# Optimization experiments

Hardware: AMD Instinct MI355X
Metric: run time of the kernel (lower is better)

The kernel has to match this reference:

```python
import jax, jax.numpy as jnp
import numpy as np

N_LAYERS = 3
NUM_NODES = 400000
EMB_DIM = 64
N_EDGES = 4000000


def setup_inputs() -> dict:
    key = jax.random.key(0)
    k1, k2, k3, k4 = jax.random.split(key, 4)
    embedding = jax.random.normal(k1, (NUM_NODES, EMB_DIM), dtype=jnp.float32) * 0.1
    adj_row = jax.random.randint(k2, (N_EDGES,), 0, NUM_NODES, dtype=jnp.int64)
    adj_col = jax.random.randint(k3, (N_EDGES,), 0, NUM_NODES, dtype=jnp.int64)
    # normalized adjacency values (e.g. 1/sqrt(d_i d_j)); positive, small
    adj_val = jax.random.uniform(k4, (N_EDGES,), dtype=jnp.float32) * 0.01
    return {"embedding": embedding, "adj_row": adj_row, "adj_col": adj_col, "adj_val": adj_val}


def _spmm(row, col, val, x):
    # sparse [N,N] @ dense [N,D]: gather neighbor rows, scale, scatter-add
    msgs = val[:, None] * x[col]                      # [E, D]
    return jax.ops.segment_sum(msgs, row, num_segments=NUM_NODES)


def reference(embedding, adj_row, adj_col, adj_val):
    # LightGCN propagation: running mean over layer outputs (fused accumulator,
    # mathematically identical to stack+mean over n_layers+1 embeddings)
    x = embedding
    acc = x
    for _ in range(N_LAYERS):
        x = _spmm(adj_row, adj_col, adj_val, x)
        acc = acc + x
    all_embeddings = acc / jnp.asarray(N_LAYERS + 1, dtype=x.dtype)
    return all_embeddings
```

## Files before the change

### kernel.cpp

```cpp
#include <hip/hip_runtime.h>

#define EMB 64
#define SCAN_B 256
#define RPB 32
#define RPW 8
#define ECAP 1024

typedef unsigned uint2v __attribute__((ext_vector_type(2)));
typedef float float4v __attribute__((ext_vector_type(4)));

__device__ inline uint2 nt_load_u2(const uint2* p) {
    uint2v v = __builtin_nontemporal_load((const uint2v*)p);
    return make_uint2(v.x, v.y);
}
__device__ inline void nt_store_u2(uint2* p, uint2 v) {
    uint2v t; t.x = v.x; t.y = v.y;
    __builtin_nontemporal_store(t, (uint2v*)p);
}
__device__ inline float4 nt_load_f4(const float4* p) {
    float4v v = __builtin_nontemporal_load((const float4v*)p);
    return make_float4(v.x, v.y, v.z, v.w);
}
__device__ inline void nt_store_f4(float4* p, float4 v) {
    float4v t; t.x = v.x; t.y = v.y; t.z = v.z; t.w = v.w;
    __builtin_nontemporal_store(t, (float4v*)p);
}

__device__ inline unsigned short f2bf(float f) {
    unsigned u = __float_as_uint(f);
    return (unsigned short)((u + 0x7fffu + ((u >> 16) & 1u)) >> 16);
}
__device__ inline float bl(unsigned u) { return __uint_as_float(u << 16); }
__device__ inline float bh(unsigned u) { return __uint_as_float(u & 0xffff0000u); }


__global__ void zero_ints(int* __restrict__ p, int n) {
    int i = blockIdx.x * blockDim.x + threadIdx.x;
    if (i < n) p[i] = 0;
}

__global__ void hist_rows(const int* __restrict__ row, int* __restrict__ S, int E) {
    int e = blockIdx.x * blockDim.x + threadIdx.x;
    if (e < E) atomicAdd(&S[__builtin_nontemporal_load(row + e)], 1);
}

__global__ void scan_block_sums(const int* __restrict__ S, int* __restrict__ bsum, int N) {
    __shared__ int sdata[SCAN_B];
    int i = blockIdx.x * SCAN_B + threadIdx.x;
    sdata[threadIdx.x] = (i < N) ? S[i] : 0;
    __syncthreads();
    for (int off = SCAN_B / 2; off > 0; off >>= 1) {
        if (threadIdx.x < off) sdata[threadIdx.x] += sdata[threadIdx.x + off];
        __syncthreads();
    }
    if (threadIdx.x == 0) bsum[blockIdx.x] = sdata[0];
}

__global__ void scan_sums(int* __restrict__ bsum, int nb) {
    __shared__ int part[1024];
    int t = threadIdx.x;
    int i0 = 2 * t, i1 = 2 * t + 1;
    int a = (i0 < nb) ? bsum[i0] : 0;
    int b = (i1 < nb) ? bsum[i1] : 0;
    part[t] = a + b;
    __syncthreads();
    for (int off = 1; off < 1024; off <<= 1) {
        int v = part[t];
        int add = (t >= off) ? part[t - off] : 0;
        __syncthreads();
        part[t] = v + add;
        __syncthreads();
    }
    int excl = (t == 0) ? 0 : part[t - 1];
    if (i0 < nb) bsum[i0] = excl;
    if (i1 < nb) bsum[i1] = excl + a;
}

__global__ void scan_apply(int* __restrict__ S, const int* __restrict__ bsum, int N) {
    __shared__ int sdata[SCAN_B];
    int i = blockIdx.x * SCAN_B + threadIdx.x;
    int v = (i < N) ? S[i] : 0;
    sdata[threadIdx.x] = v;
    __syncthreads();
    for (int off = 1; off < SCAN_B; off <<= 1) {
        int val = sdata[threadIdx.x];
        int add = (threadIdx.x >= off) ? sdata[threadIdx.x - off] : 0;
        __syncthreads();
        sdata[threadIdx.x] = val + add;
        __syncthreads();
    }
    int excl = (threadIdx.x == 0 ? 0 : sdata[threadIdx.x - 1]) + bsum[blockIdx.x];
    if (i < N) S[i] = excl;
}

__global__ void scatter_edges_ranged(const int* __restrict__ row, const int* __restrict__ col,
                                     const float* __restrict__ val,
                                     int* __restrict__ S, uint2* __restrict__ epack,
                                     int E, int rstep) {
    int pass  = blockIdx.x & 7;
    int chunk = blockIdx.x >> 3;
    int e = chunk * blockDim.x + threadIdx.x;
    if (e >= E) return;
    int r = __builtin_nontemporal_load(row + e);
    int lo = pass * rstep;
    if (r < lo || r >= lo + rstep) return;
    int c = __builtin_nontemporal_load(col + e);
    float v = __builtin_nontemporal_load(val + e);
    int pos = atomicAdd(&S[r], 1);
    epack[pos] = make_uint2((unsigned)c, __float_as_uint(v));
}

__global__ void conv_bf16(const float4* __restrict__ src, uint2* __restrict__ dst, int n4) {
    int i = blockIdx.x * blockDim.x + threadIdx.x;
    if (i < n4) {
        float4 v = nt_load_f4(src + i);
        unsigned w0 = (unsigned)f2bf(v.x) | ((unsigned)f2bf(v.y) << 16);
        unsigned w1 = (unsigned)f2bf(v.z) | ((unsigned)f2bf(v.w) << 16);
        nt_store_u2(dst + i, make_uint2(w0, w1));
    }
}

template<bool STG>
__device__ __forceinline__ void spmm_rows(
    const uint2* __restrict__ epack, const uint2* __restrict__ esh, int beg0,
    const int* __restrict__ Ssh, int j0,
    const unsigned short* __restrict__ x, const float* __restrict__ emb,
    unsigned short* __restrict__ y, float* __restrict__ acc,
    int rb, int N, int mode, int lane, int grp, int d4)
{
    const uint2 z2 = make_uint2(0u, 0u);

#define EDG(i) (STG ? esh[(i) - beg0] : epack[i])
#define LOADR(J, B_, E_, P0, P1, P2, P3, G0, G1, G2, G3)                         \
    {                                                                            \
        B_ = Ssh[J]; E_ = Ssh[(J) + 1];                                          \
        int i0 = B_ + grp, i1 = i0 + 4, i2 = i0 + 8, i3 = i0 + 12;               \
        P0 = (i0 < E_) ? EDG(i0) : z2;                                           \
        P1 = (i1 < E_) ? EDG(i1) : z2;                                           \
        P2 = (i2 < E_) ? EDG(i2) : z2;                                           \
        P3 = (i3 < E_) ? EDG(i3) : z2;                                           \
        G0 = (i0 < E_) ? ((const uint2*)(x + ((size_t)P0.x << 6)))[d4] : z2;     \
        G1 = (i1 < E_) ? ((const uint2*)(x + ((size_t)P1.x << 6)))[d4] : z2;     \
        G2 = (i2 < E_) ? ((const uint2*)(x + ((size_t)P2.x << 6)))[d4] : z2;     \
        G3 = (i3 < E_) ? ((const uint2*)(x + ((size_t)P3.x << 6)))[d4] : z2;     \
    }

    int aB = 0, aE = 0;
    uint2 ap0 = z2, ap1 = z2, ap2 = z2, ap3 = z2, ag0 = z2, ag1 = z2, ag2 = z2, ag3 = z2;
    int bB = 0, bE = 0;
    uint2 bp0 = z2, bp1 = z2, bp2 = z2, bp3 = z2, bg0 = z2, bg1 = z2, bg2 = z2, bg3 = z2;

    LOADR(j0, aB, aE, ap0, ap1, ap2, ap3, ag0, ag1, ag2, ag3);

    for (int k = 0; k < RPW; ++k) {
        int j = j0 + k;
        int r = rb + j;
        if (k + 1 < RPW) {
            LOADR(j + 1, bB, bE, bp0, bp1, bp2, bp3, bg0, bg1, bg2, bg3);
        }

        float4 s = make_float4(0.f, 0.f, 0.f, 0.f);
        {
            int i0 = aB + grp, i1 = i0 + 4, i2 = i0 + 8, i3 = i0 + 12;
            float w0 = (i0 < aE) ? __uint_as_float(ap0.y) : 0.f;
            float w1 = (i1 < aE) ? __uint_as_float(ap1.y) : 0.f;
            float w2 = (i2 < aE) ? __uint_as_float(ap2.y) : 0.f;
            float w3 = (i3 < aE) ? __uint_as_float(ap3.y) : 0.f;
            s.x += w0 * bl(ag0.x); s.y += w0 * bh(ag0.x); s.z += w0 * bl(ag0.y); s.w += w0 * bh(ag0.y);
            s.x += w1 * bl(ag1.x); s.y += w1 * bh(ag1.x); s.z += w1 * bl(ag1.y); s.w += w1 * bh(ag1.y);
            s.x += w2 * bl(ag2.x); s.y += w2 * bh(ag2.x); s.z += w2 * bl(ag2.y); s.w += w2 * bh(ag2.y);
            s.x += w3 * bl(ag3.x); s.y += w3 * bh(ag3.x); s.z += w3 * bl(ag3.y); s.w += w3 * bh(ag3.y);
        }
        for (int base = aB + 16; base < aE; base += 16) {
            int i0 = base + grp, i1 = i0 + 4, i2 = i0 + 8, i3 = i0 + 12;
            uint2 p0 = (i0 < aE) ? EDG(i0) : z2;
            uint2 p1 = (i1 < aE) ? EDG(i1) : z2;
            uint2 p2 = (i2 < aE) ? EDG(i2) : z2;
            uint2 p3 = (i3 < aE) ? EDG(i3) : z2;
            uint2 g0 = (i0 < aE) ? ((const uint2*)(x + ((size_t)p0.x << 6)))[d4] : z2;
            uint2 g1 = (i1 < aE) ? ((const uint2*)(x + ((size_t)p1.x << 6)))[d4] : z2;
            uint2 g2 = (i2 < aE) ? ((const uint2*)(x + ((size_t)p2.x << 6)))[d4] : z2;
            uint2 g3 = (i3 < aE) ? ((const uint2*)(x + ((size_t)p3.x << 6)))[d4] : z2;
            float w0 = (i0 < aE) ? __uint_as_float(p0.y) : 0.f;
            float w1 = (i1 < aE) ? __uint_as_float(p1.y) : 0.f;
            float w2 = (i2 < aE) ? __uint_as_float(p2.y) : 0.f;
            float w3 = (i3 < aE) ? __uint_as_float(p3.y) : 0.f;
            s.x += w0 * bl(g0.x); s.y += w0 * bh(g0.x); s.z += w0 * bl(g0.y); s.w += w0 * bh(g0.y);
            s.x += w1 * bl(g1.x); s.y += w1 * bh(g1.x); s.z += w1 * bl(g1.y); s.w += w1 * bh(g1.y);
            s.x += w2 * bl(g2.x); s.y += w2 * bh(g2.x); s.z += w2 * bl(g2.y); s.w += w2 * bh(g2.y);
            s.x += w3 * bl(g3.x); s.y += w3 * bh(g3.x); s.z += w3 * bl(g3.y); s.w += w3 * bh(g3.y);
        }

        s.x += __shfl_xor(s.x, 32); s.y += __shfl_xor(s.y, 32);
        s.z += __shfl_xor(s.z, 32); s.w += __shfl_xor(s.w, 32);
        s.x += __shfl_xor(s.x, 16); s.y += __shfl_xor(s.y, 16);
        s.z += __shfl_xor(s.z, 16); s.w += __shfl_xor(s.w, 16);

        if (lane < 16 && r < N) {
            size_t o4 = (size_t)r * 16 + d4;
            if (mode != 2) {
                unsigned w0 = (unsigned)f2bf(s.x) | ((unsigned)f2bf(s.y) << 16);
                unsigned w1 = (unsigned)f2bf(s.z) | ((unsigned)f2bf(s.w) << 16);
                nt_store_u2(((uint2*)y) + o4, make_uint2(w0, w1));
            }
            if (mode == 0) {
                float4 e4 = nt_load_f4(((const float4*)emb) + o4);
                nt_store_f4(((float4*)acc) + o4,
                            make_float4(e4.x + s.x, e4.y + s.y, e4.z + s.z, e4.w + s.w));
            } else if (mode == 1) {
                float4 a4 = nt_load_f4(((const float4*)acc) + o4);
                nt_store_f4(((float4*)acc) + o4,
                            make_float4(a4.x + s.x, a4.y + s.y, a4.z + s.z, a4.w + s.w));
            } else if (mode == 2) {
                float4 a4 = nt_load_f4(((const float4*)acc) + o4);
                nt_store_f4(((float4*)acc) + o4,
                            make_float4((a4.x + s.x) * 0.25f, (a4.y + s.y) * 0.25f,
                                        (a4.z + s.z) * 0.25f, (a4.w + s.w) * 0.25f));
            }
        }
        aB = bB; aE = bE;
        ap0 = bp0; ap1 = bp1; ap2 = bp2; ap3 = bp3;
        ag0 = bg0; ag1 = bg1; ag2 = bg2; ag3 = bg3;
    }
#undef LOADR
#undef EDG
}

__global__ __launch_bounds__(256) void spmm_csr2(
    const uint2* __restrict__ epack, const int* __restrict__ S,
    const unsigned short* __restrict__ x, const float* __restrict__ emb,
    unsigned short* __restrict__ y, float* __restrict__ acc,
    int N, int mode)
{
    __shared__ int Ssh[RPB + 1];
    __shared__ uint2 esh[ECAP];

    int tid = threadIdx.x;
    int rb = blockIdx.x * RPB;

    if (tid <= RPB) {
        int rr = rb - 1 + tid;
        Ssh[tid] = (rr < 0) ? 0 : S[rr < N ? rr : (N - 1)];
    }
    __syncthreads();

    int beg0 = Ssh[0];
    int nE = Ssh[RPB] - beg0;
    bool staged = (nE <= ECAP);
    if (staged) {
        for (int i = tid; i < nE; i += 256) esh[i] = nt_load_u2(epack + beg0 + i);
    }
    __syncthreads();

    int wid = tid >> 6, lane = tid & 63;
    int grp = lane >> 4, d4 = lane & 15;
    int j0 = wid * RPW;

    if (staged)
        spmm_rows<true >(epack, esh, beg0, Ssh, j0, x, emb, y, acc, rb, N, mode, lane, grp, d4);
    else
        spmm_rows<false>(epack, esh, beg0, Ssh, j0, x, emb, y, acc, rb, N, mode, lane, grp, d4);
}


__global__ void lgcn_init(const float4* __restrict__ emb, float4* __restrict__ A,
                          float4* __restrict__ acc, float4* __restrict__ B, int n4) {
    int i = blockIdx.x * blockDim.x + threadIdx.x;
    if (i < n4) { float4 v = emb[i]; A[i] = v; acc[i] = v; B[i] = make_float4(0,0,0,0); }
}
__global__ void lgcn_spmm(const int* __restrict__ row, const int* __restrict__ col,
                          const float* __restrict__ val, const float* __restrict__ x,
                          float* __restrict__ y, int E) {
    int gid = blockIdx.x * blockDim.x + threadIdx.x;
    int e = gid >> 6;
    if (e >= E) return;
    int d = threadIdx.x & 63;
    atomicAdd(y + (size_t)row[e] * EMB + d, val[e] * x[(size_t)col[e] * EMB + d]);
}
__global__ void lgcn_addzero(float4* __restrict__ acc, const float4* __restrict__ X,
                             float4* __restrict__ Y, int n4) {
    int i = blockIdx.x * blockDim.x + threadIdx.x;
    if (i < n4) {
        float4 a = acc[i]; float4 xv = X[i];
        a.x += xv.x; a.y += xv.y; a.z += xv.z; a.w += xv.w;
        acc[i] = a; Y[i] = make_float4(0,0,0,0);
    }
}
__global__ void lgcn_final(float4* __restrict__ acc, const float4* __restrict__ X, int n4) {
    int i = blockIdx.x * blockDim.x + threadIdx.x;
    if (i < n4) {
        float4 a = acc[i]; float4 xv = X[i];
        a.x = (a.x + xv.x) * 0.25f; a.y = (a.y + xv.y) * 0.25f;
        a.z = (a.z + xv.z) * 0.25f; a.w = (a.w + xv.w) * 0.25f;
        acc[i] = a;
    }
}

extern "C" void kernel_launch(void* const* d_in, const int* in_sizes, int n_in,
                              void* d_out, int out_size, void* d_ws, size_t ws_size,
                              hipStream_t stream) {
    const float* emb = (const float*)d_in[0];
    const int*   row = (const int*)d_in[1];
    const int*   col = (const int*)d_in[2];
    const float* val = (const float*)d_in[3];
    float* acc = (float*)d_out;

    const int N = in_sizes[0] / EMB;
    const int E = in_sizes[1];
    const int TB = 256;

    const size_t buf_elems = (size_t)N * EMB;
    const int nb = (N + SCAN_B - 1) / SCAN_B;

    const size_t need = (size_t)E * 8 + buf_elems * 2 * 3 + (size_t)N * 4 + (size_t)nb * 4;

    if (ws_size >= need) {
        uint2* epack = (uint2*)d_ws;
        unsigned short* X0 = (unsigned short*)(epack + E);
        unsigned short* X1 = X0 + buf_elems;
        unsigned short* X2 = X1 + buf_elems;
        int* S    = (int*)(X2 + buf_elems);
        int* bsum = S + N;

        const int eb  = (E + TB - 1) / TB;
        const int nbN = (N + TB - 1) / TB;
        const int n4  = (int)(buf_elems / 4);
        const int cvb = (n4 + TB - 1) / TB;
        const int spmm_blocks = (N + RPB - 1) / RPB;
        const int rstep = (N + 7) / 8;

        zero_ints<<<nbN, TB, 0, stream>>>(S, N);
        hist_rows<<<eb, TB, 0, stream>>>(row, S, E);
        scan_block_sums<<<nb, SCAN_B, 0, stream>>>(S, bsum, N);
        scan_sums<<<1, 1024, 0, stream>>>(bsum, nb);
        scan_apply<<<nb, SCAN_B, 0, stream>>>(S, bsum, N);
        scatter_edges_ranged<<<eb * 8, TB, 0, stream>>>(row, col, val, S, epack, E, rstep);
        conv_bf16<<<cvb, TB, 0, stream>>>((const float4*)emb, (uint2*)X0, n4);

        spmm_csr2<<<spmm_blocks, TB, 0, stream>>>(epack, S, X0, emb, X1, acc, N, 0);
        spmm_csr2<<<spmm_blocks, TB, 0, stream>>>(epack, S, X1, nullptr, X2, acc, N, 1);
        spmm_csr2<<<spmm_blocks, TB, 0, stream>>>(epack, S, X2, nullptr, nullptr, acc, N, 2);
    } else {
        float* A = (float*)d_ws;
        float* B = A + buf_elems;
        const int n4 = (int)(buf_elems / 4);
        const int ew_blocks = (n4 + TB - 1) / TB;
        const int spmm_blocks = (E + 3) / 4;
        lgcn_init<<<ew_blocks, TB, 0, stream>>>((const float4*)emb, (float4*)A,
                                                (float4*)acc, (float4*)B, n4);
        lgcn_spmm<<<spmm_blocks, TB, 0, stream>>>(row, col, val, A, B, E);
        lgcn_addzero<<<ew_blocks, TB, 0, stream>>>((float4*)acc, (const float4*)B,
                                                   (float4*)A, n4);
        lgcn_spmm<<<spmm_blocks, TB, 0, stream>>>(row, col, val, B, A, E);
        lgcn_addzero<<<ew_blocks, TB, 0, stream>>>((float4*)acc, (const float4*)A,
                                                   (float4*)B, n4);
        lgcn_spmm<<<spmm_blocks, TB, 0, stream>>>(row, col, val, A, B, E);
        lgcn_final<<<ew_blocks, TB, 0, stream>>>((float4*)acc, (const float4*)B, n4);
    }
}
```

Before: 1.050 ms.

## Defer accumulator to final layer and vectorize row histogram

The first two SpMM passes now write only the bf16 layer outputs. The fp32 accumulator is built once in the last pass from emb, the two stored bf16 layer buffers and the final sum, which removes two full fp32 read-modify-write sweeps over acc. The row histogram also loads four row indices per thread with one 128-bit nontemporal load. The trade-off is that layers 1 and 2 enter the accumulator at bf16 precision instead of fp32, which adds rounding error.

New measurement: 982.2 us (median of 2 runs). 1.07x faster.

```diff
diff --git a/kernel.cpp b/kernel.cpp
--- a/kernel.cpp
+++ b/kernel.cpp
@@ -8,6 +8,7 @@
 
 typedef unsigned uint2v __attribute__((ext_vector_type(2)));
 typedef float float4v __attribute__((ext_vector_type(4)));
+typedef int int4v __attribute__((ext_vector_type(4)));
 
 __device__ inline uint2 nt_load_u2(const uint2* p) {
     uint2v v = __builtin_nontemporal_load((const uint2v*)p);
@@ -42,6 +43,17 @@
 __global__ void hist_rows(const int* __restrict__ row, int* __restrict__ S, int E) {
     int e = blockIdx.x * blockDim.x + threadIdx.x;
     if (e < E) atomicAdd(&S[__builtin_nontemporal_load(row + e)], 1);
+}
+
+__global__ void hist_rows4(const int* __restrict__ row, int* __restrict__ S, int E4) {
+    int i = blockIdx.x * blockDim.x + threadIdx.x;
+    if (i < E4) {
+        int4v r = __builtin_nontemporal_load((const int4v*)row + i);
+        atomicAdd(&S[r.x], 1);
+        atomicAdd(&S[r.y], 1);
+        atomicAdd(&S[r.z], 1);
+        atomicAdd(&S[r.w], 1);
+    }
 }
 
 __global__ void scan_block_sums(const int* __restrict__ S, int* __restrict__ bsum, int N) {
@@ -125,6 +137,7 @@
     const uint2* __restrict__ epack, const uint2* __restrict__ esh, int beg0,
     const int* __restrict__ Ssh, int j0,
     const unsigned short* __restrict__ x, const float* __restrict__ emb,
+    const uint2* __restrict__ x1b, const uint2* __restrict__ x2b,
     unsigned short* __restrict__ y, float* __restrict__ acc,
     int rb, int N, int mode, int lane, int grp, int d4)
 {
@@ -202,20 +215,16 @@
                 unsigned w0 = (unsigned)f2bf(s.x) | ((unsigned)f2bf(s.y) << 16);
                 unsigned w1 = (unsigned)f2bf(s.z) | ((unsigned)f2bf(s.w) << 16);
                 nt_store_u2(((uint2*)y) + o4, make_uint2(w0, w1));
-            }
-            if (mode == 0) {
+            } else {
                 float4 e4 = nt_load_f4(((const float4*)emb) + o4);
+                uint2 a1 = nt_load_u2(x1b + o4);
+                uint2 a2 = nt_load_u2(x2b + o4);
+                float rx = e4.x + bl(a1.x) + bl(a2.x) + s.x;
+                float ry = e4.y + bh(a1.x) + bh(a2.x) + s.y;
+                float rz = e4.z + bl(a1.y) + bl(a2.y) + s.z;
+                float rw = e4.w + bh(a1.y) + bh(a2.y) + s.w;
                 nt_store_f4(((float4*)acc) + o4,
-                            make_float4(e4.x + s.x, e4.y + s.y, e4.z + s.z, e4.w + s.w));
-            } else if (mode == 1) {
-                float4 a4 = nt_load_f4(((const float4*)acc) + o4);
-                nt_store_f4(((float4*)acc) + o4,
-                            make_float4(a4.x + s.x, a4.y + s.y, a4.z + s.z, a4.w + s.w));
-            } else if (mode == 2) {
-                float4 a4 = nt_load_f4(((const float4*)acc) + o4);
-                nt_store_f4(((float4*)acc) + o4,
-                            make_float4((a4.x + s.x) * 0.25f, (a4.y + s.y) * 0.25f,
-                                        (a4.z + s.z) * 0.25f, (a4.w + s.w) * 0.25f));
+                            make_float4(rx * 0.25f, ry * 0.25f, rz * 0.25f, rw * 0.25f));
             }
         }
         aB = bB; aE = bE;
@@ -229,6 +238,7 @@
 __global__ __launch_bounds__(256) void spmm_csr2(
     const uint2* __restrict__ epack, const int* __restrict__ S,
     const unsigned short* __restrict__ x, const float* __restrict__ emb,
+    const uint2* __restrict__ x1b, const uint2* __restrict__ x2b,
     unsigned short* __restrict__ y, float* __restrict__ acc,
     int N, int mode)
 {
@@ -257,9 +267,9 @@
     int j0 = wid * RPW;
 
     if (staged)
-        spmm_rows<true >(epack, esh, beg0, Ssh, j0, x, emb, y, acc, rb, N, mode, lane, grp, d4);
+        spmm_rows<true >(epack, esh, beg0, Ssh, j0, x, emb, x1b, x2b, y, acc, rb, N, mode, lane, grp, d4);
     else
-        spmm_rows<false>(epack, esh, beg0, Ssh, j0, x, emb, y, acc, rb, N, mode, lane, grp, d4);
+        spmm_rows<false>(epack, esh, beg0, Ssh, j0, x, emb, x1b, x2b, y, acc, rb, N, mode, lane, grp, d4);
 }
 
 
@@ -330,16 +340,25 @@
         const int rstep = (N + 7) / 8;
 
         zero_ints<<<nbN, TB, 0, stream>>>(S, N);
-        hist_rows<<<eb, TB, 0, stream>>>(row, S, E);
+        if ((E & 3) == 0) {
+            const int e4b = (E / 4 + TB - 1) / TB;
+            hist_rows4<<<e4b, TB, 0, stream>>>(row, S, E / 4);
+        } else {
+            hist_rows<<<eb, TB, 0, stream>>>(row, S, E);
+        }
         scan_block_sums<<<nb, SCAN_B, 0, stream>>>(S, bsum, N);
         scan_sums<<<1, 1024, 0, stream>>>(bsum, nb);
         scan_apply<<<nb, SCAN_B, 0, stream>>>(S, bsum, N);
         scatter_edges_ranged<<<eb * 8, TB, 0, stream>>>(row, col, val, S, epack, E, rstep);
         conv_bf16<<<cvb, TB, 0, stream>>>((const float4*)emb, (uint2*)X0, n4);
 
-        spmm_csr2<<<spmm_blocks, TB, 0, stream>>>(epack, S, X0, emb, X1, acc, N, 0);
-        spmm_csr2<<<spmm_blocks, TB, 0, stream>>>(epack, S, X1, nullptr, X2, acc, N, 1);
-        spmm_csr2<<<spmm_blocks, TB, 0, stream>>>(epack, S, X2, nullptr, nullptr, acc, N, 2);
+        spmm_csr2<<<spmm_blocks, TB, 0, stream>>>(epack, S, X0, nullptr, nullptr, nullptr,
+                                                  X1, nullptr, N, 0);
+        spmm_csr2<<<spmm_blocks, TB, 0, stream>>>(epack, S, X1, nullptr, nullptr, nullptr,
+                                                  X2, nullptr, N, 1);
+        spmm_csr2<<<spmm_blocks, TB, 0, stream>>>(epack, S, X2, emb,
+                                                  (const uint2*)X1, (const uint2*)X2,
+                                                  nullptr, acc, N, 2);
     } else {
         float* A = (float*)d_ws;
         float* B = A + buf_elems;
```
